# Performance work log

Hardware: AMD Instinct MI355X
Metric: run time of the kernel (lower is better)

## Reference

```python
import jax, jax.numpy as jnp
import numpy as np

LAYER_SIZE, STACK_SIZE = 10, 4
RES_C, SKIP_C = 128, 128
B, T = 4, 8192
DILATIONS = [2 ** l for l in range(LAYER_SIZE)] * STACK_SIZE  # 40 blocks
N_BLOCKS = len(DILATIONS)


def setup_inputs() -> dict:
    key = jax.random.key(0)
    ks = jax.random.split(key, 6)
    s = 0.05  # weight scale to keep activations sane
    return {
        "x": jax.random.normal(ks[0], (B, RES_C, T), jnp.float32),
        # dilated causal conv weights [n_blocks, out, in, k=2], no bias
        "w_dil": jax.random.normal(ks[1], (N_BLOCKS, RES_C, RES_C, 2), jnp.float32) * s,
        # 1x1 residual conv weights/bias
        "w_res": jax.random.normal(ks[2], (N_BLOCKS, RES_C, RES_C), jnp.float32) * s,
        "b_res": jax.random.normal(ks[3], (N_BLOCKS, RES_C), jnp.float32) * s,
        # 1x1 skip conv weights/bias
        "w_skip": jax.random.normal(ks[4], (N_BLOCKS, SKIP_C, RES_C), jnp.float32) * s,
        "b_skip": jax.random.normal(ks[5], (N_BLOCKS, SKIP_C), jnp.float32) * s,
        "skip_size": 4096,
    }


def reference(x, w_dil, w_res, b_res, w_skip, b_skip, skip_size):
    out = x
    skips = []
    for i, d in enumerate(DILATIONS):
        Tc = out.shape[2]
        # dilated causal conv, kernel=2: y[t] = W0 @ x[t] + W1 @ x[t+d], out length Tc-d
        y = (jnp.einsum('oi,bit->bot', w_dil[i, :, :, 0], out[:, :, : Tc - d])
             + jnp.einsum('oi,bit->bot', w_dil[i, :, :, 1], out[:, :, d:]))
        gated = jnp.tanh(y) * jax.nn.sigmoid(y)
        res = jnp.einsum('oi,bit->bot', w_res[i], gated) + b_res[i][None, :, None]
        out = res + out[:, :, -res.shape[2]:]  # residual add on trimmed input
        skip = jnp.einsum('oi,bit->bot', w_skip[i], gated) + b_skip[i][None, :, None]
        skips.append(skip[:, :, -skip_size:])
    return jnp.stack(skips)  # [n_blocks, B, SKIP_C, skip_size]
```

## Files before the change

kernel.cpp:

```cpp
#include <hip/hip_runtime.h>

typedef __attribute__((ext_vector_type(8))) short bf16x8;
typedef __attribute__((ext_vector_type(4))) short bf16x4;
typedef __attribute__((ext_vector_type(4))) float f32x4;

#define TFULL 8192
#define RC 128
#define NB 40
#define BATCH 4
#define SKIP_SZ 4096

#define LDS3(p) ((__attribute__((address_space(3))) void*)(p))
#define GLB1(p) ((const __attribute__((address_space(1))) void*)(p))

#define XPLANE 16384
#define LDS_BYTES (3 * XPLANE)

__device__ __forceinline__ unsigned short f2bf(float f) {
    unsigned u = __builtin_bit_cast(unsigned, f);
    u += 0x7FFFu + ((u >> 16) & 1u);
    return (unsigned short)(u >> 16);
}
__device__ __forceinline__ float bf2f(unsigned short h) {
    unsigned u = ((unsigned)h) << 16;
    return __builtin_bit_cast(float, u);
}
__device__ __forceinline__ float gatef(float y) {
    float yc = fminf(fmaxf(y, -30.f), 30.f);
    float e  = __expf(-yc);
    float e2 = e * e;
    return (1.f - e2) * __builtin_amdgcn_rcpf(1.f + e2)
                      * __builtin_amdgcn_rcpf(1.f + e);
}

__global__ __launch_bounds__(256) void prepass(
    const float* __restrict__ x,
    const float* __restrict__ Wd, const float* __restrict__ Wr, const float* __restrict__ Ws,
    unsigned short* __restrict__ Xh, unsigned short* __restrict__ Xl,
    unsigned short* __restrict__ Wdh,
    unsigned short* __restrict__ Wrh,
    unsigned short* __restrict__ Wsh)
{
    __shared__ float t[32][65];
    const int bx  = blockIdx.x;
    const int tid = threadIdx.x;
    if (bx < 2048) {
        const int col0 = (bx & 127) * 64;
        const int ch0  = ((bx >> 7) & 3) * 32;
        const int b    = bx >> 9;
        const int tx = tid & 63, ty = tid >> 6;
#pragma unroll
        for (int i = 0; i < 8; ++i) {
            int ch = ty + i * 4;
            t[ch][tx] = x[((size_t)(b * RC + ch0 + ch)) * TFULL + col0 + tx];
        }
        __syncthreads();
        for (int idx = tid; idx < 64 * 32; idx += 256) {
            int col = idx >> 5, ch = idx & 31;
            float v = t[ch][col];
            unsigned short h = f2bf(v);
            unsigned short l = f2bf(v - bf2f(h));
            size_t off = ((size_t)(b * TFULL + col0 + col)) * RC + ch0 + ch;
            Xh[off] = h;
            Xl[off] = l;
        }
        return;
    }
    const int Nd = NB * 4096;
    const int Nr = NB * 2048;
    int id = (bx - 2048) * 256 + tid;
    const float* src;
    unsigned short* dh;
    int blk, rloc;
    bool dil = false;
    size_t dbase;
    if (id < Nd)               { dil = true; blk = id >> 12; rloc = id & 4095; dh = Wdh; src = Wd; dbase = (size_t)id * 8; }
    else if (id < Nd + Nr)     { int u = id - Nd;      blk = u >> 11; rloc = u & 2047; dh = Wrh; src = Wr; dbase = (size_t)u * 8; }
    else if (id < Nd + 2 * Nr) { int u = id - Nd - Nr; blk = u >> 11; rloc = u & 2047; dh = Wsh; src = Ws; dbase = (size_t)u * 8; }
    else return;
    const int ks = rloc >> 9, mf = (rloc >> 6) & 7, lane = rloc & 63;
    const int m = mf * 16 + (lane & 15);
    const int kb = ks * 32 + ((lane >> 4) << 3);
    bf16x8 hv;
#pragma unroll
    for (int j = 0; j < 8; ++j) {
        int k = kb + j;
        float w;
        if (dil) {
            int tap = k >> 7, i = k & 127;
            w = src[((((size_t)blk * 128 + m) * 128) + i) * 2 + tap];
        } else {
            w = src[(((size_t)blk * 128 + m) * 128) + k];
        }
        hv[j] = (short)f2bf(w);
    }
    *(bf16x8*)(dh + dbase) = hv;
}

__global__ __launch_bounds__(512, 4) void wn_step(
    const unsigned short* __restrict__ curh, const unsigned short* __restrict__ curl,
    unsigned short* __restrict__ nxth, unsigned short* __restrict__ nxtl,
    const unsigned short* __restrict__ Wdh_i,
    const unsigned short* __restrict__ Wrh_i,
    const unsigned short* __restrict__ Wsh_i,
    const float* __restrict__ br, const float* __restrict__ bs,
    float* __restrict__ skip, int d, int col0)
{
    __shared__ char lds[LDS_BYTES];

    const int tid  = threadIdx.x;
    const int lane = tid & 63;
    const int wave = tid >> 6;
    const int l15  = lane & 15, lq = lane >> 4;
    const int u    = blockIdx.x;
    const int b    = u & 3;
    const int tile0 = col0 + (u >> 2) * 64;
    const size_t xbase = (size_t)b * TFULL * RC;

#pragma unroll
    for (int r = 0; r < 4; ++r) {
        const int j   = wave * 4 + r;
        const int tap = j >> 4;
        const int c4  = (j & 15) * 4;
        const int col = c4 + lq;
        const int chs = l15 ^ (col & 7);
        int cg_ = tile0 + col;
        cg_ = cg_ > TFULL - 1 ? TFULL - 1 : cg_;
        if (!tap) cg_ -= d;
        const unsigned short* gsrc = curh + xbase + (size_t)cg_ * RC + chs * 8;
        char* ldst = lds + tap * XPLANE + c4 * 256;
        __builtin_amdgcn_global_load_lds(GLB1(gsrc), LDS3(ldst), 16, 0, 0);
    }
    __syncthreads();

    f32x4 acc[4];
#pragma unroll
    for (int nf = 0; nf < 4; ++nf) acc[nf] = (f32x4){0.f, 0.f, 0.f, 0.f};

#pragma unroll
    for (int ks = 0; ks < 8; ++ks) {
        const int tap = ks >> 2;
        const int kk  = ks & 3;
        const size_t wi = ((size_t)(ks * 8 + wave) * 64 + lane) * 8;
        bf16x8 ah = *(const bf16x8*)(Wdh_i + wi);
#pragma unroll
        for (int nf = 0; nf < 4; ++nf) {
            const int col = nf * 16 + l15;
            const int byo = (kk * 64 + lq * 16) ^ ((col & 7) << 4);
            bf16x8 bh = *(const bf16x8*)(lds + tap * XPLANE + col * 256 + byo);
            acc[nf] = __builtin_amdgcn_mfma_f32_16x16x32_bf16(ah, bh, acc[nf], 0, 0, 0);
        }
    }

    const int ch0 = wave * 16 + lq * 4;
#pragma unroll
    for (int nf = 0; nf < 4; ++nf) {
        const int n   = nf * 16 + l15;
        const int byo = (ch0 * 2) ^ ((n & 7) << 4);
        bf16x4 hv;
#pragma unroll
        for (int r = 0; r < 4; ++r)
            hv[r] = (short)f2bf(gatef(acc[nf][r]));
        *(bf16x4*)(lds + 2 * XPLANE + n * 256 + byo) = hv;
    }
    __syncthreads();

    f32x4 accr[4], accs[4];
#pragma unroll
    for (int nf = 0; nf < 4; ++nf) {
        accr[nf] = (f32x4){0.f, 0.f, 0.f, 0.f};
        accs[nf] = (f32x4){0.f, 0.f, 0.f, 0.f};
    }
#pragma unroll
    for (int ks = 0; ks < 4; ++ks) {
        const size_t wi = ((size_t)(ks * 8 + wave) * 64 + lane) * 8;
        bf16x8 rh = *(const bf16x8*)(Wrh_i + wi);
        bf16x8 sh = *(const bf16x8*)(Wsh_i + wi);
#pragma unroll
        for (int nf = 0; nf < 4; ++nf) {
            const int col = nf * 16 + l15;
            const int byo = (ks * 64 + lq * 16) ^ ((col & 7) << 4);
            bf16x8 g = *(const bf16x8*)(lds + 2 * XPLANE + col * 256 + byo);
            accr[nf] = __builtin_amdgcn_mfma_f32_16x16x32_bf16(rh, g, accr[nf], 0, 0, 0);
            accs[nf] = __builtin_amdgcn_mfma_f32_16x16x32_bf16(sh, g, accs[nf], 0, 0, 0);
        }
    }

    const int nt = TFULL - tile0 < 64 ? TFULL - tile0 : 64;
    const float4 brv = *(const float4*)(br + ch0);
    const float4 bsv = *(const float4*)(bs + ch0);
#pragma unroll
    for (int nf = 0; nf < 4; ++nf) {
        const int n = nf * 16 + l15;
        if (n < nt) {
            const int c = tile0 + n;
            const int byo = (ch0 * 2) ^ ((n & 7) << 4);
            bf16x4 ih = *(const bf16x4*)(lds + XPLANE + n * 256 + byo);
            const size_t off = xbase + (size_t)c * RC + ch0;
            bf16x4 il = *(const bf16x4*)(curl + off);
            bf16x4 oh, ol;
            float sk[4];
#pragma unroll
            for (int r = 0; r < 4; ++r) {
                float inv = bf2f((unsigned short)ih[r]) + bf2f((unsigned short)il[r]);
                float rv = accr[nf][r] + ((const float*)&brv)[r] + inv;
                unsigned short h = f2bf(rv);
                oh[r] = (short)h;
                ol[r] = (short)f2bf(rv - bf2f(h));
                sk[r] = accs[nf][r] + ((const float*)&bsv)[r];
            }
            *(bf16x4*)(nxth + off) = oh;
            *(bf16x4*)(nxtl + off) = ol;
            if (c >= TFULL - SKIP_SZ) {
                float* sp = skip + ((size_t)b * RC + ch0) * SKIP_SZ + (c - (TFULL - SKIP_SZ));
#pragma unroll
                for (int r = 0; r < 4; ++r) sp[(size_t)r * SKIP_SZ] = sk[r];
            }
        }
    }
}

template<int RXC, int STGHB>
__device__ __forceinline__ void stage_x(char* lds, const unsigned short* __restrict__ curh,
                                        size_t xbase, int t0)
{
    const int tid  = threadIdx.x;
    const int lane = tid & 63;
    const int wave = tid >> 6;
    const int l15  = lane & 15, lq = lane >> 4;
#pragma unroll
    for (int j = wave; j < RXC / 4; j += 8) {
        const int c4  = j * 4;
        const int col = c4 + lq;
        const int chs = l15 ^ (col & 7);
        int g = t0 - STGHB + col;
        g = g < 0 ? 0 : (g > TFULL - 1 ? TFULL - 1 : g);
        const unsigned short* gsrc = curh + xbase + (size_t)g * RC + chs * 8;
        __builtin_amdgcn_global_load_lds(GLB1(gsrc), LDS3(lds + c4 * 256), 16, 0, 0);
    }
}

template<int NF, int Q0v, int Q1v, int HI, bool FIRST, bool LAST>
__device__ __forceinline__ void wn_sub(
    char* lds, const int srcOff, const int dstOff,
    const unsigned short* __restrict__ Wdh_i,
    const unsigned short* __restrict__ Wrh_i,
    const unsigned short* __restrict__ Wsh_i,
    const float* __restrict__ br, const float* __restrict__ bs,
    const unsigned short* __restrict__ curl,
    unsigned short* __restrict__ nxth, unsigned short* __restrict__ nxtl,
    float* __restrict__ skip, int t0, int b, int nt)
{
    constexpr int FH = HI >> 4;
    const int tid  = threadIdx.x;
    const int lane = tid & 63;
    const int wave = tid >> 6;
    const int l15  = lane & 15, lq = lane >> 4;
    const int ch0  = wave * 16 + lq * 4;
    const size_t xbase = (size_t)b * TFULL * RC;

    f32x4 a[NF];
#pragma unroll
    for (int nf = 0; nf < NF; ++nf) a[nf] = (f32x4){0.f, 0.f, 0.f, 0.f};
#pragma unroll
    for (int ks = 0; ks < 8; ++ks) {
        const int tap = ks >> 2;
        const int kk  = ks & 3;
        const size_t wi = ((size_t)(ks * 8 + wave) * 64 + lane) * 8;
        bf16x8 ah = *(const bf16x8*)(Wdh_i + wi);
#pragma unroll
        for (int nf = 0; nf < NF; ++nf) {
            const int pc  = nf * 16 + l15 + (tap ? Q1v : Q0v);
            const int byo = pc * 256 + ((kk * 64 + lq * 16) ^ ((pc & 7) << 4));
            bf16x8 bh = *(const bf16x8*)(lds + srcOff + byo);
            a[nf] = __builtin_amdgcn_mfma_f32_16x16x32_bf16(ah, bh, a[nf], 0, 0, 0);
        }
    }

#pragma unroll
    for (int nf = 0; nf < NF; ++nf) {
        const int gc  = nf * 16 + l15;
        const int byo = gc * 256 + ((ch0 * 2) ^ ((gc & 7) << 4));
        bf16x4 hv;
#pragma unroll
        for (int r = 0; r < 4; ++r)
            hv[r] = (short)f2bf(gatef(a[nf][r]));
        *(bf16x4*)(lds + dstOff + byo) = hv;
    }
    __syncthreads();

    f32x4 rr[NF], ss[NF];
#pragma unroll
    for (int nf = 0; nf < NF; ++nf) {
        rr[nf] = (f32x4){0.f, 0.f, 0.f, 0.f};
        ss[nf] = (f32x4){0.f, 0.f, 0.f, 0.f};
    }
#pragma unroll
    for (int ks = 0; ks < 4; ++ks) {
        const size_t wi = ((size_t)(ks * 8 + wave) * 64 + lane) * 8;
        bf16x8 rh = *(const bf16x8*)(Wrh_i + wi);
        bf16x8 sh = *(const bf16x8*)(Wsh_i + wi);
#pragma unroll
        for (int nf = 0; nf < NF; ++nf) {
            const int gc  = nf * 16 + l15;
            const int byo = gc * 256 + ((ks * 64 + lq * 16) ^ ((gc & 7) << 4));
            bf16x8 g = *(const bf16x8*)(lds + dstOff + byo);
            rr[nf] = __builtin_amdgcn_mfma_f32_16x16x32_bf16(rh, g, rr[nf], 0, 0, 0);
            ss[nf] = __builtin_amdgcn_mfma_f32_16x16x32_bf16(sh, g, ss[nf], 0, 0, 0);
        }
    }
    __syncthreads();

    const float4 brv = *(const float4*)(br + ch0);
    const float4 bsv = *(const float4*)(bs + ch0);
#pragma unroll
    for (int nf = 0; nf < NF; ++nf) {
        const int yc = nf * 16 + l15;
        const int c  = t0 - HI + yc;
        const int pc = yc + Q1v;
        bf16x4 ph = *(const bf16x4*)(lds + srcOff + pc * 256 + ((ch0 * 2) ^ ((pc & 7) << 4)));
        float resid[4];
#pragma unroll
        for (int r = 0; r < 4; ++r) resid[r] = bf2f((unsigned short)ph[r]);
        if constexpr (FIRST) {
            int cg = c < 0 ? 0 : (c > TFULL - 1 ? TFULL - 1 : c);
            bf16x4 xl = *(const bf16x4*)(curl + xbase + (size_t)cg * RC + ch0);
#pragma unroll
            for (int r = 0; r < 4; ++r) resid[r] += bf2f((unsigned short)xl[r]);
        }
        float yv[4], sk[4];
#pragma unroll
        for (int r = 0; r < 4; ++r) {
            yv[r] = rr[nf][r] + ((const float*)&brv)[r] + resid[r];
            sk[r] = ss[nf][r] + ((const float*)&bsv)[r];
        }
        if constexpr (LAST) {
            const int lc = yc;
            if (lc < nt) {
                bf16x4 oh, ol;
#pragma unroll
                for (int r = 0; r < 4; ++r) {
                    unsigned short h = f2bf(yv[r]);
                    oh[r] = (short)h;
                    ol[r] = (short)f2bf(yv[r] - bf2f(h));
                }
                const size_t off = xbase + (size_t)c * RC + ch0;
                *(bf16x4*)(nxth + off) = oh;
                *(bf16x4*)(nxtl + off) = ol;
                if (c >= TFULL - SKIP_SZ) {
                    float* sp = skip + ((size_t)b * RC + ch0) * SKIP_SZ + (c - (TFULL - SKIP_SZ));
#pragma unroll
                    for (int r = 0; r < 4; ++r) sp[(size_t)r * SKIP_SZ] = sk[r];
                }
            }
        } else {
            bf16x4 yh4;
#pragma unroll
            for (int r = 0; r < 4; ++r)
                yh4[r] = (short)f2bf(yv[r]);
            *(bf16x4*)(lds + dstOff + yc * 256 + ((ch0 * 2) ^ ((yc & 7) << 4))) = yh4;
            if (nf >= FH) {
                const int lc = yc - HI;
                if (lc < nt && c >= TFULL - SKIP_SZ) {
                    float* sp = skip + ((size_t)b * RC + ch0) * SKIP_SZ + (c - (TFULL - SKIP_SZ));
#pragma unroll
                    for (int r = 0; r < 4; ++r) sp[(size_t)r * SKIP_SZ] = sk[r];
                }
            }
        }
    }
}

__global__ __launch_bounds__(512, 4) void wn_quint(
    const unsigned short* __restrict__ curh, const unsigned short* __restrict__ curl,
    unsigned short* __restrict__ nxth, unsigned short* __restrict__ nxtl,
    const unsigned short* __restrict__ Wdh,
    const unsigned short* __restrict__ Wrh,
    const unsigned short* __restrict__ Wsh,
    const float* __restrict__ br_all, const float* __restrict__ bs_all,
    float* __restrict__ out, int blk, int col0)
{
    constexpr int STGHB = 68, RXC = 132;
    constexpr int RB = RXC * 256;
    __shared__ char lds[RB + 8 * 16 * 256];

    const int u  = blockIdx.x;
    const int b  = u & 3;
    const int t0 = col0 + (u >> 2) * 64;
    const size_t xbase = (size_t)b * TFULL * RC;
    const int nt = TFULL - t0 < 64 ? TFULL - t0 : 64;
    const size_t SKB = (size_t)BATCH * RC * SKIP_SZ;

    stage_x<RXC, STGHB>(lds, curh, xbase, t0);
    __syncthreads();

#define WQ(j) Wdh + (size_t)(blk+j)*32768, \
              Wrh + (size_t)(blk+j)*16384, \
              Wsh + (size_t)(blk+j)*16384, \
              br_all + (size_t)(blk+j)*RC, bs_all + (size_t)(blk+j)*RC, \
              curl, nxth, nxtl, out + (size_t)(blk+j)*SKB, t0, b, nt

    wn_sub<8,  3,  4, 64, true,  false>(lds, 0,  RB, WQ(0));
    __syncthreads();
    wn_sub<7, 14, 16, 48, false, false>(lds, RB, 0,  WQ(1));
    __syncthreads();
    wn_sub<6, 12, 16, 32, false, false>(lds, 0,  RB, WQ(2));
    __syncthreads();
    wn_sub<5,  8, 16, 16, false, false>(lds, RB, 0,  WQ(3));
    __syncthreads();
    wn_sub<4,  0, 16,  0, false, true >(lds, 0,  RB, WQ(4));
#undef WQ
}

__global__ __launch_bounds__(512, 4) void wn_pair2(
    const unsigned short* __restrict__ curh, const unsigned short* __restrict__ curl,
    unsigned short* __restrict__ nxth, unsigned short* __restrict__ nxtl,
    const unsigned short* __restrict__ Wdh,
    const unsigned short* __restrict__ Wrh,
    const unsigned short* __restrict__ Wsh,
    const float* __restrict__ br_all, const float* __restrict__ bs_all,
    float* __restrict__ out, int blk, int col0)
{
    constexpr int STGHB = 96, RXC = 160;
    constexpr int RB = RXC * 256;
    __shared__ char lds[RB + 8 * 16 * 256];

    const int u  = blockIdx.x;
    const int b  = u & 3;
    const int t0 = col0 + (u >> 2) * 64;
    const size_t xbase = (size_t)b * TFULL * RC;
    const int nt = TFULL - t0 < 64 ? TFULL - t0 : 64;
    const size_t SKB = (size_t)BATCH * RC * SKIP_SZ;

    stage_x<RXC, STGHB>(lds, curh, xbase, t0);
    __syncthreads();

#define WQ(j) Wdh + (size_t)(blk+j)*32768, \
              Wrh + (size_t)(blk+j)*16384, \
              Wsh + (size_t)(blk+j)*16384, \
              br_all + (size_t)(blk+j)*RC, bs_all + (size_t)(blk+j)*RC, \
              curl, nxth, nxtl, out + (size_t)(blk+j)*SKB, t0, b, nt

    wn_sub<8, 0, 32, 64, true,  false>(lds, 0,  RB, WQ(0));
    __syncthreads();
    wn_sub<4, 0, 64,  0, false, true >(lds, RB, 0,  WQ(1));
#undef WQ
}

extern "C" void kernel_launch(void* const* d_in, const int* in_sizes, int n_in,
                              void* d_out, int out_size, void* d_ws, size_t ws_size,
                              hipStream_t stream) {
    const float* x  = (const float*)d_in[0];
    const float* Wd = (const float*)d_in[1];
    const float* Wr = (const float*)d_in[2];
    const float* br = (const float*)d_in[3];
    const float* Ws = (const float*)d_in[4];
    const float* bs = (const float*)d_in[5];
    float* out = (float*)d_out;

    const size_t SLOT = (size_t)BATCH * TFULL * RC;
    unsigned short* Xs0h = (unsigned short*)d_ws;
    unsigned short* Xs0l = Xs0h + SLOT;
    unsigned short* Xs1h = Xs0l + SLOT;
    unsigned short* Xs1l = Xs1h + SLOT;
    unsigned short* Wdh = Xs1l + SLOT;
    unsigned short* Wrh = Wdh + (size_t)NB * 32768;
    unsigned short* Wsh = Wrh + (size_t)NB * 16384;

    prepass<<<dim3(3328), dim3(256), 0, stream>>>(
        x, Wd, Wr, Ws, Xs0h, Xs0l, Wdh, Wrh, Wsh);

    int L = TFULL;
    int pp = 0;
    for (int s = 0; s < 4; ++s) {
        {
            const int i = s * 10;
            const int Lout = L - 31;
            const int col0 = TFULL - Lout;
            const int units = ((Lout + 63) >> 6) * BATCH;
            unsigned short* curh = pp ? Xs1h : Xs0h;
            unsigned short* curl = pp ? Xs1l : Xs0l;
            unsigned short* nxth = pp ? Xs0h : Xs1h;
            unsigned short* nxtl = pp ? Xs0l : Xs1l;
            wn_quint<<<dim3(units), dim3(512), 0, stream>>>(
                curh, curl, nxth, nxtl, Wdh, Wrh, Wsh, br, bs, out, i, col0);
            pp ^= 1;
            L = Lout;
        }
        {
            const int i = s * 10 + 5;
            const int Lout = L - 96;
            const int col0 = TFULL - Lout;
            const int units = ((Lout + 63) >> 6) * BATCH;
            unsigned short* curh = pp ? Xs1h : Xs0h;
            unsigned short* curl = pp ? Xs1l : Xs0l;
            unsigned short* nxth = pp ? Xs0h : Xs1h;
            unsigned short* nxtl = pp ? Xs0l : Xs1l;
            wn_pair2<<<dim3(units), dim3(512), 0, stream>>>(
                curh, curl, nxth, nxtl, Wdh, Wrh, Wsh, br, bs, out, i, col0);
            pp ^= 1;
            L = Lout;
        }
        for (int q = 7; q < 10; ++q) {
            const int i = s * 10 + q;
            const int d = 1 << q;
            const int Lout = L - d;
            const int col0 = TFULL - Lout;
            const int units = ((Lout + 63) >> 6) * BATCH;
            unsigned short* curh = pp ? Xs1h : Xs0h;
            unsigned short* curl = pp ? Xs1l : Xs0l;
            unsigned short* nxth = pp ? Xs0h : Xs1h;
            unsigned short* nxtl = pp ? Xs0l : Xs1l;
            wn_step<<<dim3(units), dim3(512), 0, stream>>>(
                curh, curl, nxth, nxtl,
                Wdh + (size_t)i * 32768,
                Wrh + (size_t)i * 16384,
                Wsh + (size_t)i * 16384,
                br + (size_t)i * RC, bs + (size_t)i * RC,
                out + (size_t)i * BATCH * RC * SKIP_SZ, d, col0);
            pp ^= 1;
            L = Lout;
        }
    }
}
```

Measured before the change: 524.1 us.

## Use three-buffer LDS rotation in quint kernel with tighter halo and fewer syncs

The five-block fused kernel now rotates among three LDS buffers (source, gated, output) instead of two. This removes one barrier per sub-block because the residual output no longer overwrites the gated buffer still being read. The dilation/halo parameters are re-tuned to a much smaller staged window (96 columns with a 31-column halo instead of 132/68), which cuts staging traffic and redundant halo compute per tile. LDS footprint changes, which may affect occupancy. Skip writes now use an explicit lc>=0 guard instead of an nf threshold.

```diff
diff --git a/kernel.cpp b/kernel.cpp
--- a/kernel.cpp
+++ b/kernel.cpp
@@ -240,9 +240,9 @@
     }
 }
 
-template<int NF, int Q0v, int Q1v, int HI, bool FIRST, bool LAST>
+template<int NF, int Q0v, int Q1v, int HI, bool FIRST, bool LAST, bool SEPY>
 __device__ __forceinline__ void wn_sub(
-    char* lds, const int srcOff, const int dstOff,
+    char* lds, const int srcOff, const int gOff, const int yOff,
     const unsigned short* __restrict__ Wdh_i,
     const unsigned short* __restrict__ Wrh_i,
     const unsigned short* __restrict__ Wsh_i,
@@ -251,7 +251,6 @@
     unsigned short* __restrict__ nxth, unsigned short* __restrict__ nxtl,
     float* __restrict__ skip, int t0, int b, int nt)
 {
-    constexpr int FH = HI >> 4;
     const int tid  = threadIdx.x;
     const int lane = tid & 63;
     const int wave = tid >> 6;
@@ -285,7 +284,7 @@
 #pragma unroll
         for (int r = 0; r < 4; ++r)
             hv[r] = (short)f2bf(gatef(a[nf][r]));
-        *(bf16x4*)(lds + dstOff + byo) = hv;
+        *(bf16x4*)(lds + gOff + byo) = hv;
     }
     __syncthreads();
 
@@ -304,12 +303,12 @@
         for (int nf = 0; nf < NF; ++nf) {
             const int gc  = nf * 16 + l15;
             const int byo = gc * 256 + ((ks * 64 + lq * 16) ^ ((gc & 7) << 4));
-            bf16x8 g = *(const bf16x8*)(lds + dstOff + byo);
+            bf16x8 g = *(const bf16x8*)(lds + gOff + byo);
             rr[nf] = __builtin_amdgcn_mfma_f32_16x16x32_bf16(rh, g, rr[nf], 0, 0, 0);
             ss[nf] = __builtin_amdgcn_mfma_f32_16x16x32_bf16(sh, g, ss[nf], 0, 0, 0);
         }
     }
-    __syncthreads();
+    if constexpr (!SEPY) __syncthreads();
 
     const float4 brv = *(const float4*)(br + ch0);
     const float4 bsv = *(const float4*)(bs + ch0);
@@ -335,8 +334,7 @@
             sk[r] = ss[nf][r] + ((const float*)&bsv)[r];
         }
         if constexpr (LAST) {
-            const int lc = yc;
-            if (lc < nt) {
+            if (yc < nt) {
                 bf16x4 oh, ol;
 #pragma unroll
                 for (int r = 0; r < 4; ++r) {
@@ -358,14 +356,12 @@
 #pragma unroll
             for (int r = 0; r < 4; ++r)
                 yh4[r] = (short)f2bf(yv[r]);
-            *(bf16x4*)(lds + dstOff + yc * 256 + ((ch0 * 2) ^ ((yc & 7) << 4))) = yh4;
-            if (nf >= FH) {
-                const int lc = yc - HI;
-                if (lc < nt && c >= TFULL - SKIP_SZ) {
-                    float* sp = skip + ((size_t)b * RC + ch0) * SKIP_SZ + (c - (TFULL - SKIP_SZ));
-#pragma unroll
-                    for (int r = 0; r < 4; ++r) sp[(size_t)r * SKIP_SZ] = sk[r];
-                }
+            *(bf16x4*)(lds + yOff + yc * 256 + ((ch0 * 2) ^ ((yc & 7) << 4))) = yh4;
+            const int lc = yc - HI;
+            if (lc >= 0 && lc < nt && c >= TFULL - SKIP_SZ) {
+                float* sp = skip + ((size_t)b * RC + ch0) * SKIP_SZ + (c - (TFULL - SKIP_SZ));
+#pragma unroll
+                for (int r = 0; r < 4; ++r) sp[(size_t)r * SKIP_SZ] = sk[r];
             }
         }
     }
@@ -380,9 +376,8 @@
     const float* __restrict__ br_all, const float* __restrict__ bs_all,
     float* __restrict__ out, int blk, int col0)
 {
-    constexpr int STGHB = 68, RXC = 132;
-    constexpr int RB = RXC * 256;
-    __shared__ char lds[RB + 8 * 16 * 256];
+    constexpr int RA = 0, RB = 26624, RCg = 53248;
+    __shared__ char lds[79872];
 
     const int u  = blockIdx.x;
     const int b  = u & 3;
@@ -391,7 +386,7 @@
     const int nt = TFULL - t0 < 64 ? TFULL - t0 : 64;
     const size_t SKB = (size_t)BATCH * RC * SKIP_SZ;
 
-    stage_x<RXC, STGHB>(lds, curh, xbase, t0);
+    stage_x<96, 31>(lds, curh, xbase, t0);
     __syncthreads();
 
 #define WQ(j) Wdh + (size_t)(blk+j)*32768, \
@@ -400,15 +395,15 @@
               br_all + (size_t)(blk+j)*RC, bs_all + (size_t)(blk+j)*RC, \
               curl, nxth, nxtl, out + (size_t)(blk+j)*SKB, t0, b, nt
 
-    wn_sub<8,  3,  4, 64, true,  false>(lds, 0,  RB, WQ(0));
-    __syncthreads();
-    wn_sub<7, 14, 16, 48, false, false>(lds, RB, 0,  WQ(1));
-    __syncthreads();
-    wn_sub<6, 12, 16, 32, false, false>(lds, 0,  RB, WQ(2));
-    __syncthreads();
-    wn_sub<5,  8, 16, 16, false, false>(lds, RB, 0,  WQ(3));
-    __syncthreads();
-    wn_sub<4,  0, 16,  0, false, true >(lds, 0,  RB, WQ(4));
+    wn_sub<6, 0,  1, 30, true,  false, true>(lds, RA,  RB,  RCg, WQ(0));
+    __syncthreads();
+    wn_sub<6, 0,  2, 28, false, false, true>(lds, RCg, RA,  RB,  WQ(1));
+    __syncthreads();
+    wn_sub<6, 0,  4, 24, false, false, true>(lds, RB,  RCg, RA,  WQ(2));
+    __syncthreads();
+    wn_sub<5, 0,  8, 16, false, false, true>(lds, RA,  RB,  RCg, WQ(3));
+    __syncthreads();
+    wn_sub<4, 0, 16,  0, false, true,  true>(lds, RCg, RA,  RA,  WQ(4));
 #undef WQ
 }
 
@@ -421,8 +416,7 @@
     const float* __restrict__ br_all, const float* __restrict__ bs_all,
     float* __restrict__ out, int blk, int col0)
 {
-    constexpr int STGHB = 96, RXC = 160;
-    constexpr int RB = RXC * 256;
+    constexpr int RB = 40960;
     __shared__ char lds[RB + 8 * 16 * 256];
 
     const int u  = blockIdx.x;
@@ -432,7 +426,7 @@
     const int nt = TFULL - t0 < 64 ? TFULL - t0 : 64;
     const size_t SKB = (size_t)BATCH * RC * SKIP_SZ;
 
-    stage_x<RXC, STGHB>(lds, curh, xbase, t0);
+    stage_x<160, 96>(lds, curh, xbase, t0);
     __syncthreads();
 
 #define WQ(j) Wdh + (size_t)(blk+j)*32768, \
@@ -441,9 +435,9 @@
               br_all + (size_t)(blk+j)*RC, bs_all + (size_t)(blk+j)*RC, \
               curl, nxth, nxtl, out + (size_t)(blk+j)*SKB, t0, b, nt
 
-    wn_sub<8, 0, 32, 64, true,  false>(lds, 0,  RB, WQ(0));
-    __syncthreads();
-    wn_sub<4, 0, 64,  0, false, true >(lds, RB, 0,  WQ(1));
+    wn_sub<8, 0, 32, 64, true,  false, false>(lds, 0,  RB, RB, WQ(0));
+    __syncthreads();
+    wn_sub<4, 0, 64,  0, false, true,  false>(lds, RB, 0,  0,  WQ(1));
 #undef WQ
 }
 
```

Measured after the change: 511.2 us. 1.03x faster.
